# Performance work log

Measured on AMD Instinct MI355X. Metric: run time of the kernel, lower is better.

## Reference

```python
import jax, jax.numpy as jnp
import numpy as np
import math

D_MODEL = 1024
N_HEAD = 16
MAX_LEN = 2048
B, T = 4, 2048


def setup_inputs() -> dict:
    key = jax.random.key(0)
    k1, k2, k3, k4 = jax.random.split(key, 4)
    scale = 1.0 / math.sqrt(D_MODEL)
    return {
        "x": jax.random.normal(k1, (B, T, D_MODEL), dtype=jnp.float32),
        "Wqkv": jax.random.normal(k2, (D_MODEL, 3 * D_MODEL), dtype=jnp.float32) * scale,
        "Wproj": jax.random.normal(k3, (D_MODEL, D_MODEL), dtype=jnp.float32) * scale,
        "rel_bias": jax.random.normal(k4, (MAX_LEN, N_HEAD), dtype=jnp.float32) * 0.02,
    }


def reference(x, Wqkv, Wproj, rel_bias):
    B, T, C = x.shape
    H = rel_bias.shape[1]
    hd = C // H
    # fused qkv projection (Linear without bias)
    qkv = x @ Wqkv                                   # [B,T,3C]
    q, k, v = jnp.split(qkv, 3, axis=-1)
    q = q.reshape(B, T, H, hd).transpose(0, 2, 1, 3)  # [B,H,T,hd]
    k = k.reshape(B, T, H, hd).transpose(0, 2, 1, 3)
    v = v.reshape(B, T, H, hd).transpose(0, 2, 1, 3)
    att = jnp.einsum("bhqd,bhkd->bhqk", q, k) * (1.0 / math.sqrt(hd))
    # relative position bias: dist[i,j] = max(i-j, 0), looked up in table
    pos = jnp.arange(T)
    dist = jnp.clip(pos[:, None] - pos[None, :], 0)   # [T,T] int
    r_bias = rel_bias[dist].transpose(2, 0, 1)        # [H,T,T]
    att = att + r_bias[None]
    # causal mask (lower-triangular allowed)
    causal = pos[:, None] >= pos[None, :]             # [T,T]
    att = jnp.where(causal[None, None], att, -jnp.inf)
    att = jax.nn.softmax(att, axis=-1)
    y = jnp.einsum("bhqk,bhkd->bhqd", att, v)         # [B,H,T,hd]
    y = y.transpose(0, 2, 1, 3).reshape(B, T, C)
    return y @ Wproj
```

## Files before the change

kernel.cpp:

```cpp
#include <hip/hip_runtime.h>
#include <hip/hip_bf16.h>

#define T_SEQ 2048
#define CDIM  1024
#define NH    16
#define HD    64
#define BATCH 4
#define MROWS (BATCH * T_SEQ)
#define QSCALE 0.18033688011112042f
#define LOG2E  1.4426950408889634f

typedef __attribute__((ext_vector_type(8))) short bf16x8;
typedef __attribute__((ext_vector_type(4))) float f32x4;

__device__ __forceinline__ ushort f2bf(float f) {
    unsigned u = __float_as_uint(f);
    unsigned r = (u + 0x7fffu + ((u >> 16) & 1u)) >> 16;
    return (ushort)r;
}

__device__ __forceinline__ ushort f2bf_hw(float f) {
    __hip_bfloat16 h = __float2bfloat16(f);
    return *reinterpret_cast<ushort*>(&h);
}

__device__ __forceinline__ void gload_lds16(const void* g, void* l) {
    __builtin_amdgcn_global_load_lds(
        (const __attribute__((address_space(1))) unsigned int*)g,
        (__attribute__((address_space(3))) unsigned int*)l, 16, 0, 0);
}

__global__ __launch_bounds__(256)
void cvt_bf16(const float* __restrict__ in, ushort* __restrict__ out, int n4)
{
    const int stride = gridDim.x * blockDim.x;
    for (int i = blockIdx.x * blockDim.x + threadIdx.x; i < n4; i += stride) {
        float4 v = *(const float4*)&in[(size_t)i * 4];
        ushort4 o;
        o.x = f2bf(v.x); o.y = f2bf(v.y); o.z = f2bf(v.z); o.w = f2bf(v.w);
        *(ushort4*)&out[(size_t)i * 4] = o;
    }
}

__global__ __launch_bounds__(256)
void transpose_cvt(const float* __restrict__ in, ushort* __restrict__ out,
                   int R, int C)
{
    __shared__ float t[32][33];
    const int c0 = blockIdx.x * 32, r0 = blockIdx.y * 32;
    const int tx = threadIdx.x & 31, ty = threadIdx.x >> 5;
    #pragma unroll
    for (int rr = 0; rr < 32; rr += 8)
        t[rr + ty][tx] = in[(size_t)(r0 + rr + ty) * C + c0 + tx];
    __syncthreads();
    #pragma unroll
    for (int rr = 0; rr < 32; rr += 8)
        out[(size_t)(c0 + rr + ty) * R + r0 + tx] = f2bf(t[tx][rr + ty]);
}

template<int SCATTER>
__global__ __launch_bounds__(256)
void gemm_mfma(const ushort* __restrict__ A, const ushort* __restrict__ Bt,
               float* __restrict__ C0, ushort* __restrict__ Q0,
               ushort* __restrict__ K0, ushort* __restrict__ V0,
               int M, int N, int K)
{
    __shared__ __align__(16) char LDSb[32768];
    char* Asm = LDSb;
    char* Bsm = LDSb + 16384;

    const int tid  = threadIdx.x;
    const int wave = tid >> 6;
    const int lane = tid & 63;
    const int lr   = lane & 15;
    const int lg   = lane >> 4;
    const int wr   = wave >> 1;
    const int wc   = wave & 1;
    const int m0   = blockIdx.x * 128;
    const int n0   = blockIdx.y * 128;

    const int prow = lane >> 3;
    const int pcb  = (lane & 7) * 16;

    const f32x4 zero4 = {0.f, 0.f, 0.f, 0.f};
    f32x4 acc[4][4];
    #pragma unroll
    for (int i = 0; i < 4; ++i)
        #pragma unroll
        for (int j = 0; j < 4; ++j) acc[i][j] = zero4;

    const char* Abase = (const char*)A;
    const char* Bbase = (const char*)Bt;

    for (int k0 = 0; k0 < K; k0 += 64) {
        __syncthreads();
        #pragma unroll
        for (int p = 0; p < 4; ++p) {
            const int row = wave * 32 + p * 8 + prow;
            const int soff = pcb ^ ((row & 7) << 4);
            gload_lds16(Abase + ((size_t)(m0 + row) * K + k0) * 2 + soff,
                        Asm + (wave * 32 + p * 8) * 128);
            gload_lds16(Bbase + ((size_t)(n0 + row) * K + k0) * 2 + soff,
                        Bsm + (wave * 32 + p * 8) * 128);
        }
        __syncthreads();

        #pragma unroll
        for (int ks = 0; ks < 2; ++ks) {
            bf16x8 af[4], bf[4];
            #pragma unroll
            for (int mt = 0; mt < 4; ++mt) {
                const int row = wr * 64 + mt * 16 + lr;
                af[mt] = *(const bf16x8*)(Asm + row * 128 +
                         ((ks * 64 + lg * 16) ^ ((row & 7) << 4)));
            }
            #pragma unroll
            for (int nt = 0; nt < 4; ++nt) {
                const int row = wc * 64 + nt * 16 + lr;
                bf[nt] = *(const bf16x8*)(Bsm + row * 128 +
                         ((ks * 64 + lg * 16) ^ ((row & 7) << 4)));
            }
            #pragma unroll
            for (int mt = 0; mt < 4; ++mt)
                #pragma unroll
                for (int nt = 0; nt < 4; ++nt)
                    acc[mt][nt] = __builtin_amdgcn_mfma_f32_16x16x32_bf16(
                        af[mt], bf[nt], acc[mt][nt], 0, 0, 0);
        }
    }

    if (SCATTER == 0) {
        #pragma unroll
        for (int mt = 0; mt < 4; ++mt)
            #pragma unroll
            for (int r4 = 0; r4 < 4; ++r4) {
                const int m = m0 + wr * 64 + mt * 16 + lg * 4 + r4;
                float* cr = C0 + (size_t)m * N + n0 + wc * 64;
                #pragma unroll
                for (int nt = 0; nt < 4; ++nt)
                    cr[nt * 16 + lr] = acc[mt][nt][r4];
            }
    } else {
        const int which = n0 >> 10;
        const int nn  = n0 & (CDIM - 1);
        const int h0  = nn >> 6;
        const int b   = m0 >> 11;
        const int t0t = m0 & (T_SEQ - 1);
        __syncthreads();
        if (which < 2) {
            const float qs = (which == 0) ? QSCALE : 1.0f;
            #pragma unroll
            for (int mt = 0; mt < 4; ++mt)
                #pragma unroll
                for (int r4 = 0; r4 < 4; ++r4) {
                    const int row = wr * 64 + mt * 16 + lg * 4 + r4;
                    char* rp = LDSb + row * 256;
                    const int swr = (row & 7) << 4;
                    #pragma unroll
                    for (int nt = 0; nt < 4; ++nt) {
                        const int col = wc * 64 + nt * 16 + lr;
                        *(ushort*)(rp + ((col * 2) ^ swr)) =
                            f2bf(acc[mt][nt][r4] * qs);
                    }
                }
            __syncthreads();
            ushort* dstb = ((which == 0) ? Q0 : K0) + (size_t)(b * NH) * T_SEQ * HD;
            #pragma unroll
            for (int it = 0; it < 8; ++it) {
                const int cid  = it * 256 + tid;
                const int row  = cid >> 4;
                const int colb = (cid & 15) * 16;
                int4 vdat = *(const int4*)(LDSb + row * 256 +
                                           (colb ^ ((row & 7) << 4)));
                const int col = colb >> 1;
                const int h   = h0 + (col >> 6);
                const int dc  = col & 63;
                *(int4*)&dstb[((size_t)h * T_SEQ + t0t + row) * HD + dc] = vdat;
            }
        } else {
            #pragma unroll
            for (int mt = 0; mt < 4; ++mt)
                #pragma unroll
                for (int r4 = 0; r4 < 4; ++r4) {
                    const int trow = wr * 64 + mt * 16 + lg * 4 + r4;
                    #pragma unroll
                    for (int nt = 0; nt < 4; ++nt) {
                        const int col = wc * 64 + nt * 16 + lr;
                        *(ushort*)(LDSb + col * 256 +
                                   ((trow * 2) ^ ((col & 7) << 4))) =
                            f2bf(acc[mt][nt][r4]);
                    }
                }
            __syncthreads();
            ushort* vbase = V0 + (size_t)(b * NH) * HD * T_SEQ;
            #pragma unroll
            for (int it = 0; it < 8; ++it) {
                const int cid = it * 256 + tid;
                const int col = cid >> 4;
                const int tb  = (cid & 15) * 16;
                int4 vdat = *(const int4*)(LDSb + col * 256 +
                                           (tb ^ ((col & 7) << 4)));
                const int h = h0 + (col >> 6);
                const int d = col & 63;
                *(int4*)&vbase[((size_t)h * HD + d) * T_SEQ + t0t + (tb >> 1)] = vdat;
            }
        }
    }
}

__global__ __launch_bounds__(512, 4)
void attn_mfma(const ushort* __restrict__ qb, const ushort* __restrict__ kb,
               const ushort* __restrict__ vb, const float* __restrict__ rb,
               ushort* __restrict__ y)
{
    __shared__ __align__(16) char KsB[64 * 128];
    __shared__ __align__(16) char VtB[64 * 128];
    __shared__ __align__(16) char PsB[8][16 * 128];
    __shared__ float rbs[T_SEQ];

    const int tid  = threadIdx.x;
    const int wave = tid >> 6;
    const int lane = tid & 63;
    const int lr   = lane & 15;
    const int lg   = lane >> 4;
    const int bh   = blockIdx.x;
    const int h    = bh & (NH - 1);
    const int b    = bh >> 4;
    const int qtA  = 15 - (int)blockIdx.y;
    const int qtB  = (int)blockIdx.y;

    for (int i = tid; i < qtA * 128 + 128; i += 512)
        rbs[i] = rb[(size_t)i * NH + h] * LOG2E;

    const char* kbp = (const char*)(kb + (size_t)bh * T_SEQ * HD);
    const char* vbp = (const char*)(vb + (size_t)bh * HD * T_SEQ);

    const int r_st  = tid >> 3;
    const int cb    = (tid & 7) * 16;
    const int sw_st = (r_st & 7) << 4;

    const f32x4 zero4 = {0.f, 0.f, 0.f, 0.f};
    const short onebf = (short)0x3F80;
    const bf16x8 ones = {onebf, onebf, onebf, onebf, onebf, onebf, onebf, onebf};

    #pragma unroll 1
    for (int pass = 0; pass < 2; ++pass) {
        const int qt = pass ? qtB : qtA;
        const int q0 = qt * 128;
        const int nkt = 2 * (qt + 1);

        const ushort* qrow = qb + ((size_t)bh * T_SEQ + q0 + wave * 16 + lr) * HD;
        const bf16x8 aq0 = *(const bf16x8*)(qrow + lg * 8);
        const bf16x8 aq1 = *(const bf16x8*)(qrow + 32 + lg * 8);

        f32x4 Oa[4] = {zero4, zero4, zero4, zero4};
        f32x4 lacc = zero4;

        int4 kreg = *(const int4*)(kbp + (size_t)r_st * HD * 2 + cb);
        int4 vreg = *(const int4*)(vbp + (size_t)r_st * T_SEQ * 2 + cb);

        for (int kt = 0; kt < nkt; ++kt) {
            const int j0 = kt * 64;
            __syncthreads();
            *(int4*)(KsB + r_st * 128 + (cb ^ sw_st)) = kreg;
            *(int4*)(VtB + r_st * 128 + (cb ^ sw_st)) = vreg;
            __syncthreads();
            if (kt + 1 < nkt) {
                const int j1 = j0 + 64;
                kreg = *(const int4*)(kbp + (size_t)(j1 + r_st) * HD * 2 + cb);
                vreg = *(const int4*)(vbp + ((size_t)r_st * T_SEQ + j1) * 2 + cb);
            }

            f32x4 sa[4] = {zero4, zero4, zero4, zero4};
            #pragma unroll
            for (int nt = 0; nt < 4; ++nt) {
                const int row = nt * 16 + lr;
                const int sw  = (row & 7) << 4;
                bf16x8 bk0 = *(const bf16x8*)(KsB + row * 128 + ((lg * 16) ^ sw));
                bf16x8 bk1 = *(const bf16x8*)(KsB + row * 128 + ((64 + lg * 16) ^ sw));
                sa[nt] = __builtin_amdgcn_mfma_f32_16x16x32_bf16(aq0, bk0, sa[nt], 0, 0, 0);
                sa[nt] = __builtin_amdgcn_mfma_f32_16x16x32_bf16(aq1, bk1, sa[nt], 0, 0, 0);
            }

            const bool interior = (j0 + 63) <= (q0 + wave * 16);
            if (interior) {
                #pragma unroll
                for (int r4 = 0; r4 < 4; ++r4) {
                    const int gi = q0 + wave * 16 + lg * 4 + r4;
                    const int prow = lg * 4 + r4;
                    char* pw = PsB[wave] + prow * 128;
                    const int swp = (prow & 7) << 4;
                    #pragma unroll
                    for (int nt = 0; nt < 4; ++nt) {
                        const int gj = j0 + nt * 16 + lr;
                        const float p = exp2f(sa[nt][r4] + rbs[gi - gj]);
                        *(ushort*)(pw + (((nt * 16 + lr) * 2) ^ swp)) = f2bf_hw(p);
                    }
                }
            } else {
                #pragma unroll
                for (int r4 = 0; r4 < 4; ++r4) {
                    const int gi = q0 + wave * 16 + lg * 4 + r4;
                    const int prow = lg * 4 + r4;
                    char* pw = PsB[wave] + prow * 128;
                    const int swp = (prow & 7) << 4;
                    #pragma unroll
                    for (int nt = 0; nt < 4; ++nt) {
                        const int gj = j0 + nt * 16 + lr;
                        const float p = (gj <= gi)
                            ? exp2f(sa[nt][r4] + rbs[gi - gj]) : 0.0f;
                        *(ushort*)(pw + (((nt * 16 + lr) * 2) ^ swp)) = f2bf_hw(p);
                    }
                }
            }

            bf16x8 ap0 = *(const bf16x8*)(PsB[wave] + lr * 128 + ((lg * 16) ^ ((lr & 7) << 4)));
            bf16x8 ap1 = *(const bf16x8*)(PsB[wave] + lr * 128 + ((64 + lg * 16) ^ ((lr & 7) << 4)));
            lacc = __builtin_amdgcn_mfma_f32_16x16x32_bf16(ap0, ones, lacc, 0, 0, 0);
            lacc = __builtin_amdgcn_mfma_f32_16x16x32_bf16(ap1, ones, lacc, 0, 0, 0);
            #pragma unroll
            for (int dt = 0; dt < 4; ++dt) {
                const int row = dt * 16 + lr;
                const int sw  = (row & 7) << 4;
                bf16x8 bv0 = *(const bf16x8*)(VtB + row * 128 + ((lg * 16) ^ sw));
                bf16x8 bv1 = *(const bf16x8*)(VtB + row * 128 + ((64 + lg * 16) ^ sw));
                Oa[dt] = __builtin_amdgcn_mfma_f32_16x16x32_bf16(ap0, bv0, Oa[dt], 0, 0, 0);
                Oa[dt] = __builtin_amdgcn_mfma_f32_16x16x32_bf16(ap1, bv1, Oa[dt], 0, 0, 0);
            }
        }

        #pragma unroll
        for (int r4 = 0; r4 < 4; ++r4) {
            const float inv = 1.0f / lacc[r4];
            const int t = q0 + wave * 16 + lg * 4 + r4;
            ushort* yr = y + ((size_t)(b * T_SEQ + t)) * CDIM + h * HD;
            #pragma unroll
            for (int dt = 0; dt < 4; ++dt) yr[dt * 16 + lr] = f2bf_hw(Oa[dt][r4] * inv);
        }
        __syncthreads();
    }
}

extern "C" void kernel_launch(void* const* d_in, const int* in_sizes, int n_in,
                              void* d_out, int out_size, void* d_ws, size_t ws_size,
                              hipStream_t stream)
{
    const float* x     = (const float*)d_in[0];
    const float* Wqkv  = (const float*)d_in[1];
    const float* Wproj = (const float*)d_in[2];
    const float* rb    = (const float*)d_in[3];
    float* out = (float*)d_out;

    const size_t per = (size_t)BATCH * NH * T_SEQ * HD;
    ushort* xb  = (ushort*)d_ws;
    ushort* wqT = xb + per;
    ushort* wpT = wqT + (size_t)3 * CDIM * CDIM;
    ushort* qw  = wpT + (size_t)CDIM * CDIM;
    ushort* kw  = qw + per;
    ushort* vw  = kw + per;
    ushort* yb  = vw + per;
    const size_t need = (per * 5 + (size_t)4 * CDIM * CDIM) * sizeof(ushort);
    if (ws_size < need) return;

    cvt_bf16<<<2048, 256, 0, stream>>>(x, xb, (int)(per / 4));
    transpose_cvt<<<dim3(3 * CDIM / 32, CDIM / 32), 256, 0, stream>>>(Wqkv, wqT, CDIM, 3 * CDIM);
    transpose_cvt<<<dim3(CDIM / 32, CDIM / 32), 256, 0, stream>>>(Wproj, wpT, CDIM, CDIM);

    dim3 g1(MROWS / 128, (3 * CDIM) / 128);
    gemm_mfma<1><<<g1, dim3(256), 0, stream>>>(xb, wqT, nullptr, qw, kw, vw,
                                               MROWS, 3 * CDIM, CDIM);

    dim3 g2(BATCH * NH, 8);
    attn_mfma<<<g2, dim3(512), 0, stream>>>(qw, kw, vw, rb, yb);

    dim3 g3(MROWS / 128, CDIM / 128);
    gemm_mfma<0><<<g3, dim3(256), 0, stream>>>(yb, wpT, out, nullptr, nullptr, nullptr,
                                               MROWS, CDIM, CDIM);
}
```

Measured before the change: 180.4 us.

## Double-buffer K/V tiles in LDS with a single barrier per iteration

After: 181.8 us. About the same (+0.8%).

```diff
diff --git a/kernel.cpp b/kernel.cpp
--- a/kernel.cpp
+++ b/kernel.cpp
@@ -213,10 +213,11 @@
                const ushort* __restrict__ vb, const float* __restrict__ rb,
                ushort* __restrict__ y)
 {
-    __shared__ __align__(16) char KsB[64 * 128];
-    __shared__ __align__(16) char VtB[64 * 128];
-    __shared__ __align__(16) char PsB[8][16 * 128];
-    __shared__ float rbs[T_SEQ];
+    __shared__ __align__(16) char LDS[57344];
+    char*  KsB = LDS;
+    char*  VtB = LDS + 16384;
+    char*  PsB = LDS + 32768;
+    float* rbs = (float*)(LDS + 49152);
 
     const int tid  = threadIdx.x;
     const int wave = tid >> 6;
@@ -258,17 +259,27 @@
 
         int4 kreg = *(const int4*)(kbp + (size_t)r_st * HD * 2 + cb);
         int4 vreg = *(const int4*)(vbp + (size_t)r_st * T_SEQ * 2 + cb);
+        *(int4*)(KsB + r_st * 128 + (cb ^ sw_st)) = kreg;
+        *(int4*)(VtB + r_st * 128 + (cb ^ sw_st)) = vreg;
+        __syncthreads();
+        kreg = *(const int4*)(kbp + (size_t)(64 + r_st) * HD * 2 + cb);
+        vreg = *(const int4*)(vbp + ((size_t)r_st * T_SEQ + 64) * 2 + cb);
 
         for (int kt = 0; kt < nkt; ++kt) {
             const int j0 = kt * 64;
-            __syncthreads();
-            *(int4*)(KsB + r_st * 128 + (cb ^ sw_st)) = kreg;
-            *(int4*)(VtB + r_st * 128 + (cb ^ sw_st)) = vreg;
-            __syncthreads();
+            const char* Kc = KsB + (kt & 1) * 8192;
+            const char* Vc = VtB + (kt & 1) * 8192;
+
             if (kt + 1 < nkt) {
-                const int j1 = j0 + 64;
-                kreg = *(const int4*)(kbp + (size_t)(j1 + r_st) * HD * 2 + cb);
-                vreg = *(const int4*)(vbp + ((size_t)r_st * T_SEQ + j1) * 2 + cb);
+                char* Kn = KsB + ((kt + 1) & 1) * 8192;
+                char* Vn = VtB + ((kt + 1) & 1) * 8192;
+                *(int4*)(Kn + r_st * 128 + (cb ^ sw_st)) = kreg;
+                *(int4*)(Vn + r_st * 128 + (cb ^ sw_st)) = vreg;
+                if (kt + 2 < nkt) {
+                    const int j2 = j0 + 128;
+                    kreg = *(const int4*)(kbp + (size_t)(j2 + r_st) * HD * 2 + cb);
+                    vreg = *(const int4*)(vbp + ((size_t)r_st * T_SEQ + j2) * 2 + cb);
+                }
             }
 
             f32x4 sa[4] = {zero4, zero4, zero4, zero4};
@@ -276,8 +287,8 @@
             for (int nt = 0; nt < 4; ++nt) {
                 const int row = nt * 16 + lr;
                 const int sw  = (row & 7) << 4;
-                bf16x8 bk0 = *(const bf16x8*)(KsB + row * 128 + ((lg * 16) ^ sw));
-                bf16x8 bk1 = *(const bf16x8*)(KsB + row * 128 + ((64 + lg * 16) ^ sw));
+                bf16x8 bk0 = *(const bf16x8*)(Kc + row * 128 + ((lg * 16) ^ sw));
+                bf16x8 bk1 = *(const bf16x8*)(Kc + row * 128 + ((64 + lg * 16) ^ sw));
                 sa[nt] = __builtin_amdgcn_mfma_f32_16x16x32_bf16(aq0, bk0, sa[nt], 0, 0, 0);
                 sa[nt] = __builtin_amdgcn_mfma_f32_16x16x32_bf16(aq1, bk1, sa[nt], 0, 0, 0);
             }
@@ -288,7 +299,7 @@
                 for (int r4 = 0; r4 < 4; ++r4) {
                     const int gi = q0 + wave * 16 + lg * 4 + r4;
                     const int prow = lg * 4 + r4;
-                    char* pw = PsB[wave] + prow * 128;
+                    char* pw = PsB + wave * 2048 + prow * 128;
                     const int swp = (prow & 7) << 4;
                     #pragma unroll
                     for (int nt = 0; nt < 4; ++nt) {
@@ -302,7 +313,7 @@
                 for (int r4 = 0; r4 < 4; ++r4) {
                     const int gi = q0 + wave * 16 + lg * 4 + r4;
                     const int prow = lg * 4 + r4;
-                    char* pw = PsB[wave] + prow * 128;
+                    char* pw = PsB + wave * 2048 + prow * 128;
                     const int swp = (prow & 7) << 4;
                     #pragma unroll
                     for (int nt = 0; nt < 4; ++nt) {
@@ -314,19 +325,21 @@
                 }
             }
 
-            bf16x8 ap0 = *(const bf16x8*)(PsB[wave] + lr * 128 + ((lg * 16) ^ ((lr & 7) << 4)));
-            bf16x8 ap1 = *(const bf16x8*)(PsB[wave] + lr * 128 + ((64 + lg * 16) ^ ((lr & 7) << 4)));
+            bf16x8 ap0 = *(const bf16x8*)(PsB + wave * 2048 + lr * 128 + ((lg * 16) ^ ((lr & 7) << 4)));
+            bf16x8 ap1 = *(const bf16x8*)(PsB + wave * 2048 + lr * 128 + ((64 + lg * 16) ^ ((lr & 7) << 4)));
             lacc = __builtin_amdgcn_mfma_f32_16x16x32_bf16(ap0, ones, lacc, 0, 0, 0);
             lacc = __builtin_amdgcn_mfma_f32_16x16x32_bf16(ap1, ones, lacc, 0, 0, 0);
             #pragma unroll
             for (int dt = 0; dt < 4; ++dt) {
                 const int row = dt * 16 + lr;
                 const int sw  = (row & 7) << 4;
-                bf16x8 bv0 = *(const bf16x8*)(VtB + row * 128 + ((lg * 16) ^ sw));
-                bf16x8 bv1 = *(const bf16x8*)(VtB + row * 128 + ((64 + lg * 16) ^ sw));
+                bf16x8 bv0 = *(const bf16x8*)(Vc + row * 128 + ((lg * 16) ^ sw));
+                bf16x8 bv1 = *(const bf16x8*)(Vc + row * 128 + ((64 + lg * 16) ^ sw));
                 Oa[dt] = __builtin_amdgcn_mfma_f32_16x16x32_bf16(ap0, bv0, Oa[dt], 0, 0, 0);
                 Oa[dt] = __builtin_amdgcn_mfma_f32_16x16x32_bf16(ap1, bv1, Oa[dt], 0, 0, 0);
             }
+
+            __syncthreads();
         }
 
         #pragma unroll
@@ -337,7 +350,6 @@
             #pragma unroll
             for (int dt = 0; dt < 4; ++dt) yr[dt * 16 + lr] = f2bf_hw(Oa[dt][r4] * inv);
         }
-        __syncthreads();
     }
 }
 
```
